# Kernel optimization log

Measured on AMD Instinct MI355X. Metric: run time of the kernel, lower is better.

## Reference

```python
import jax, jax.numpy as jnp
import numpy as np

D_MODEL = 1024
NUM_HEADS = 16
D_K = D_MODEL // NUM_HEADS


def setup_inputs() -> dict:
    key = jax.random.key(0)
    ks = jax.random.split(key, 5)
    s = 1.0 / np.sqrt(D_MODEL)
    return {
        "x": jax.random.normal(ks[0], (2, 2048, D_MODEL), dtype=jnp.float32),
        "Wq": jax.random.normal(ks[1], (D_MODEL, D_MODEL), dtype=jnp.float32) * s,
        "bq": jnp.zeros((D_MODEL,), jnp.float32),
        "Wk": jax.random.normal(ks[2], (D_MODEL, D_MODEL), dtype=jnp.float32) * s,
        "bk": jnp.zeros((D_MODEL,), jnp.float32),
        "Wv": jax.random.normal(ks[3], (D_MODEL, D_MODEL), dtype=jnp.float32) * s,
        "bv": jnp.zeros((D_MODEL,), jnp.float32),
        "Wo": jax.random.normal(ks[4], (D_MODEL, D_MODEL), dtype=jnp.float32) * s,
        "bo": jnp.zeros((D_MODEL,), jnp.float32),
    }


def _rotate_half(t):
    t1, t2 = t[..., : D_K // 2], t[..., D_K // 2 :]
    return jnp.concatenate((-t2, t1), axis=-1)


def reference(x, Wq, bq, Wk, bk, Wv, bv, Wo, bo):
    B, S, D = x.shape
    H, dk = NUM_HEADS, D_K
    # RoPE tables: inv_freq over even dims, emb = cat(freqs, freqs)
    inv_freq = 1.0 / (10000.0 ** (jnp.arange(0, dk, 2, dtype=jnp.float32) / dk))
    pos = jnp.arange(S, dtype=jnp.float32)
    freqs = pos[:, None] * inv_freq[None, :]            # [S, dk/2]
    emb = jnp.concatenate((freqs, freqs), axis=-1)      # [S, dk]
    cos = jnp.cos(emb)[None, :, None, :]                # [1, S, 1, dk]
    sin = jnp.sin(emb)[None, :, None, :]

    q = (x @ Wq + bq).reshape(B, S, H, dk)
    k = (x @ Wk + bk).reshape(B, S, H, dk)
    v = (x @ Wv + bv).reshape(B, S, H, dk)

    q = q * cos + _rotate_half(q) * sin
    k = k * cos + _rotate_half(k) * sin

    # [B,H,S,S] scores, stable softmax, then weighted sum of V
    scores = jnp.einsum("bqhd,bkhd->bhqk", q, k) / jnp.sqrt(jnp.float32(dk))
    attn = jax.nn.softmax(scores, axis=-1)
    out = jnp.einsum("bhqk,bkhd->bqhd", attn, v).reshape(B, S, D)
    return out @ Wo + bo
```

## Files before the change

### kernel.cpp

```cpp
#include <hip/hip_runtime.h>
#include <hip/hip_bf16.h>
#include <math.h>

typedef __bf16 bf16_t;
typedef bf16_t bf16x4 __attribute__((ext_vector_type(4)));
typedef bf16_t bf16x8 __attribute__((ext_vector_type(8)));
typedef float f32x4 __attribute__((ext_vector_type(4)));

#define SEQ 2048
#define BATCH 2
#define NHEAD 16
#define DK 64
#define DMODEL 1024

#define GLOAD16(gsrc, ldst)                                                        \
    __builtin_amdgcn_global_load_lds(                                              \
        (const __attribute__((address_space(1))) void*)(gsrc),                     \
        (__attribute__((address_space(3))) void*)(ldst), 16, 0, 0)

__device__ __forceinline__ float exp2_hw(float x) {
#if __has_builtin(__builtin_amdgcn_exp2f)
    return __builtin_amdgcn_exp2f(x);
#else
    float r; asm("v_exp_f32 %0, %1" : "=v"(r) : "v"(x)); return r;
#endif
}

__global__ __launch_bounds__(256)
void prep_kernel(const float* __restrict__ x, bf16_t* __restrict__ y,
                 const float* __restrict__ W0, const float* __restrict__ W1,
                 const float* __restrict__ W2, const float* __restrict__ W3,
                 bf16_t* __restrict__ Wt, float2* __restrict__ cs) {
    __shared__ float t[32][33];
    const int id = blockIdx.x, tid = threadIdx.x;
    if (id < 4096) {
        int i = (id * 256 + tid) * 4;
        float4 v = *reinterpret_cast<const float4*>(x + i);
        bf16x4 o = { (bf16_t)v.x, (bf16_t)v.y, (bf16_t)v.z, (bf16_t)v.w };
        *reinterpret_cast<bf16x4*>(y + i) = o;
    } else if (id < 8192) {
        const int id2 = id - 4096;
        const int z = id2 >> 10, rem = id2 & 1023;
        const int n0 = (rem & 31) * 32, k0 = ((rem >> 5) & 31) * 32;
        const int tx = tid & 31, ty = tid >> 5;
        const float* W = (z == 0) ? W0 : (z == 1) ? W1 : (z == 2) ? W2 : W3;
        bf16_t* out = Wt + ((size_t)z << 20);
#pragma unroll
        for (int i = 0; i < 32; i += 8)
            t[ty + i][tx] = W[(size_t)(k0 + ty + i) * DMODEL + n0 + tx];
        __syncthreads();
#pragma unroll
        for (int i = 0; i < 32; i += 8)
            out[(size_t)(n0 + ty + i) * DMODEL + k0 + tx] = (bf16_t)t[tx][ty + i];
    } else {
        int idx = (id - 8192) * 256 + tid;
        int j = idx & 31, s = idx >> 5;
        float inv = powf(10000.0f, -(float)j / 32.0f);
        float ang = (float)s * inv;
        cs[idx] = make_float2(cosf(ang), sinf(ang));
    }
}

template<int NF>
__device__ __forceinline__ void gemm_core(const bf16_t* __restrict__ A,
                                          const bf16_t* __restrict__ Bt,
                                          int m0, int n0,
                                          bf16_t* As, bf16_t* Bs,
                                          f32x4 (&acc)[4][NF]) {
    const int tid = threadIdx.x, lane = tid & 63, wid = tid >> 6;
    const int wr = wid >> 1, wc = wid & 1;
    const int lm = lane & 15, lq = lane >> 4;
    constexpr int BROWS = NF * 32;
    constexpr int NT = DMODEL / 32;

    const int r_in = lane >> 2;
    const int csw  = (((lane & 3) ^ ((lane >> 3) & 3)) << 3);
    const bf16_t* Ag = A  + (size_t)(m0 + 32 * wid + r_in) * DMODEL + csw;
    const bf16_t* Bg = Bt + (size_t)(n0 + (NF * 8) * wid + r_in) * DMODEL + csw;
    const int cswr = ((lq ^ ((lm >> 1) & 3)) << 4);

    auto stage = [&](int t, int buf) {
        const int k0 = t * 32;
        bf16_t* a = As + buf * (128 * 32) + 32 * wid * 32;
        bf16_t* b = Bs + buf * (BROWS * 32) + (NF * 8) * wid * 32;
        GLOAD16(Ag + k0,               a);
        GLOAD16(Ag + 16 * DMODEL + k0, a + 16 * 32);
        GLOAD16(Bg + k0,               b);
        if constexpr (NF == 4) GLOAD16(Bg + 16 * DMODEL + k0, b + 16 * 32);
    };

    stage(0, 0);
    stage(1, 1);
    int cb = 0;
    for (int t = 0; t < NT; ++t) {
        if (t + 2 < NT) {
            int sb = cb + 2; if (sb >= 3) sb -= 3;
            stage(t + 2, sb);
            if constexpr (NF == 4) asm volatile("s_waitcnt vmcnt(8)" ::: "memory");
            else                   asm volatile("s_waitcnt vmcnt(6)" ::: "memory");
        } else if (t + 1 < NT) {
            if constexpr (NF == 4) asm volatile("s_waitcnt vmcnt(4)" ::: "memory");
            else                   asm volatile("s_waitcnt vmcnt(3)" ::: "memory");
        } else {
            asm volatile("s_waitcnt vmcnt(0)" ::: "memory");
        }
        __builtin_amdgcn_s_barrier();

        const char* pAs = (const char*)(As + cb * (128 * 32));
        const char* pBs = (const char*)(Bs + cb * (BROWS * 32));
        bf16x8 af[4], bfr[NF];
#pragma unroll
        for (int mf = 0; mf < 4; ++mf)
            af[mf] = *reinterpret_cast<const bf16x8*>(pAs + (wr * 64 + mf * 16 + lm) * 64 + cswr);
#pragma unroll
        for (int nf = 0; nf < NF; ++nf)
            bfr[nf] = *reinterpret_cast<const bf16x8*>(pBs + (wc * (NF * 16) + nf * 16 + lm) * 64 + cswr);
#pragma unroll
        for (int mf = 0; mf < 4; ++mf)
#pragma unroll
            for (int nf = 0; nf < NF; ++nf)
                acc[mf][nf] = __builtin_amdgcn_mfma_f32_16x16x32_bf16(af[mf], bfr[nf], acc[mf][nf], 0, 0, 0);

        asm volatile("" ::: "memory");
        __builtin_amdgcn_s_barrier();
        if (++cb == 3) cb = 0;
    }
}

__global__ __launch_bounds__(256)
void gemm_qkv_kernel(const bf16_t* __restrict__ xb, const bf16_t* __restrict__ wtqk,
                     const bf16_t* __restrict__ wtv,
                     const float* __restrict__ bq, const float* __restrict__ bk,
                     const float* __restrict__ bv,
                     bf16_t* __restrict__ qb, bf16_t* __restrict__ kb,
                     bf16_t* __restrict__ vtb, const float2* __restrict__ cs) {
    __shared__ bf16_t As[3 * 128 * 32];
    __shared__ bf16_t Bs[3 * 128 * 32];
    const int tid = threadIdx.x, lane = tid & 63, wid = tid >> 6;
    const int wr = wid >> 1, wc = wid & 1;
    const int lm = lane & 15, lq = lane >> 4;
    const int orig = blockIdx.x;
    const int id = (orig & 7) * 96 + (orig >> 3);
    f32x4 acc[4][4] = {};

    if (id < 512) {
        const int m0 = (id >> 4) * 128, n0 = (id & 15) * 128;
        gemm_core<4>(xb, wtqk, m0, n0, As, Bs, acc);
        const bool is_k = (n0 >= 1024);
        const float* bs = is_k ? bk : bq;
        bf16_t* C = is_k ? kb : qb;
        const int cb = (is_k ? n0 - 1024 : n0) + wc * 64;
        const float b0 = bs[cb + lm],      b1 = bs[cb + 16 + lm];
        const float b2 = bs[cb + 32 + lm], b3 = bs[cb + 48 + lm];
#pragma unroll
        for (int mf = 0; mf < 4; ++mf)
#pragma unroll
            for (int i = 0; i < 4; ++i) {
                const int row = m0 + wr * 64 + mf * 16 + lq * 4 + i;
                const int s = row & (SEQ - 1);
                const float2 cs0 = cs[s * 32 + lm];
                const float2 cs1 = cs[s * 32 + 16 + lm];
                const float a0 = acc[mf][0][i] + b0, a1 = acc[mf][1][i] + b1;
                const float a2 = acc[mf][2][i] + b2, a3 = acc[mf][3][i] + b3;
                bf16_t* p = C + (size_t)row * DMODEL + cb;
                p[lm]      = (bf16_t)(a0 * cs0.x - a2 * cs0.y);
                p[16 + lm] = (bf16_t)(a1 * cs1.x - a3 * cs1.y);
                p[32 + lm] = (bf16_t)(a2 * cs0.x + a0 * cs0.y);
                p[48 + lm] = (bf16_t)(a3 * cs1.x + a1 * cs1.y);
            }
    } else {
        const int id2 = id - 512;
        const int m0 = (id2 & 7) * 128, n0 = (id2 >> 3) * 128;
        gemm_core<4>(wtv, xb, m0, n0, As, Bs, acc);
#pragma unroll
        for (int mf = 0; mf < 4; ++mf)
#pragma unroll
            for (int i = 0; i < 4; ++i) {
                const int row = m0 + wr * 64 + mf * 16 + lq * 4 + i;
                const float brow = bv[row];
#pragma unroll
                for (int nf = 0; nf < 4; ++nf) {
                    const int col = n0 + wc * 64 + nf * 16 + lm;
                    vtb[(size_t)row * 4096 + col] = (bf16_t)(acc[mf][nf][i] + brow);
                }
            }
    }
}

__global__ __launch_bounds__(256)
void gemm_out_kernel(const bf16_t* __restrict__ A, const bf16_t* __restrict__ Bt,
                     const float* __restrict__ bias, float* __restrict__ C) {
    __shared__ bf16_t As[3 * 128 * 32];
    __shared__ bf16_t Bs[3 * 64 * 32];
    const int tid = threadIdx.x, lane = tid & 63, wid = tid >> 6;
    const int wr = wid >> 1, wc = wid & 1;
    const int lm = lane & 15, lq = lane >> 4;
    const int orig = blockIdx.x;
    const int id = (orig & 7) * 64 + (orig >> 3);
    const int m0 = (id >> 4) * 128, n0 = (id & 15) * 64;
    f32x4 acc[4][2] = {};
    gemm_core<2>(A, Bt, m0, n0, As, Bs, acc);
#pragma unroll
    for (int nf = 0; nf < 2; ++nf) {
        const int col = n0 + wc * 32 + nf * 16 + lm;
        const float bcol = bias[col];
#pragma unroll
        for (int mf = 0; mf < 4; ++mf)
#pragma unroll
            for (int i = 0; i < 4; ++i) {
                const int row = m0 + wr * 64 + mf * 16 + lq * 4 + i;
                C[(size_t)row * DMODEL + col] = acc[mf][nf][i] + bcol;
            }
    }
}

__global__ __launch_bounds__(256)
void attn_kernel(const bf16_t* __restrict__ q, const bf16_t* __restrict__ k,
                 const bf16_t* __restrict__ vt, bf16_t* __restrict__ attnout) {
    const int tid = threadIdx.x, lane = tid & 63, wid = tid >> 6;
    const int lm = lane & 15, lq = lane >> 4;
    const int bid = blockIdx.x;
    const int xcd = bid & 7, idx = bid >> 3;
    const int bh = xcd * 4 + (idx & 3), qblk = idx >> 2;
    const int b = bh >> 4, h = bh & 15;
    const int qrow0 = qblk * 128 + wid * 32;
    const float MS = 20.0f;
    constexpr int NT = SEQ / 64;

    __shared__ bf16_t Ks[4][64][64];
    __shared__ bf16_t Vs[4][64][64];

    const bf16_t* qA = q + ((size_t)(b * SEQ + qrow0 + lm) * NHEAD + h) * DK + lq * 8;
    const bf16_t* qB = qA + (size_t)16 * NHEAD * DK;
    bf16x8 aqA0 = *reinterpret_cast<const bf16x8*>(qA);
    bf16x8 aqA1 = *reinterpret_cast<const bf16x8*>(qA + 32);
    bf16x8 aqB0 = *reinterpret_cast<const bf16x8*>(qB);
    bf16x8 aqB1 = *reinterpret_cast<const bf16x8*>(qB + 32);
#pragma unroll
    for (int j = 0; j < 8; ++j) {
        aqA0[j] = (bf16_t)((float)aqA0[j] * 0.18033688f);
        aqA1[j] = (bf16_t)((float)aqA1[j] * 0.18033688f);
        aqB0[j] = (bf16_t)((float)aqB0[j] * 0.18033688f);
        aqB1[j] = (bf16_t)((float)aqB1[j] * 0.18033688f);
    }
    const bf16_t one = (bf16_t)1.0f;
    const bf16x8 ones = { one, one, one, one, one, one, one, one };
    const f32x4 cinit = { -MS, -MS, -MS, -MS };

    const int r0   = 8 * wid + (lane >> 3);
    const int scol = (((lane & 7) ^ (lane >> 3)) << 3);
    const int sig  = ((r0 >> 2) & 3) * 8 + ((r0 >> 4) & 1) * 4 + (r0 & 3);
    const bf16_t* kg = k  + ((size_t)(b * SEQ + sig) * NHEAD + h) * DK + scol;
    const bf16_t* vg = vt + ((size_t)(h * DK + r0)) * 4096 + (size_t)b * SEQ + scol;
    const size_t kstep = (size_t)NHEAD * DK;
    const char* ksb = (const char*)Ks;
    const char* vsb = (const char*)Vs;
    const int c0 = (lq << 4) ^ ((lm & 7) << 4);
    const int rowb = lm * 128;

    f32x4 OA[4] = {}, OB[4] = {};
    f32x4 olA = {}, olB = {};

    auto stageK = [&](int buf, int kb) {
        GLOAD16(kg + (size_t)kb * kstep,        &Ks[buf][8 * wid][0]);
        GLOAD16(kg + (size_t)(kb + 32) * kstep, &Ks[buf][32 + 8 * wid][0]);
    };
    auto stageV = [&](int buf, int kb) {
        GLOAD16(vg + kb,                        &Vs[buf][8 * wid][0]);
        GLOAD16(vg + (size_t)32 * 4096 + kb,    &Vs[buf][32 + 8 * wid][0]);
    };
    auto qk = [&](int buf, f32x4 (&sA)[4], f32x4 (&sB)[4]) {
        const char* kt = ksb + buf * 8192;
        __builtin_amdgcn_s_setprio(1);
#pragma unroll
        for (int t = 0; t < 4; ++t) {
            bf16x8 a0 = *reinterpret_cast<const bf16x8*>(kt + t * 2048 + rowb + c0);
            bf16x8 a1 = *reinterpret_cast<const bf16x8*>(kt + t * 2048 + rowb + (c0 ^ 64));
            f32x4 xA = __builtin_amdgcn_mfma_f32_16x16x32_bf16(a0, aqA0, cinit, 0, 0, 0);
            xA = __builtin_amdgcn_mfma_f32_16x16x32_bf16(a1, aqA1, xA, 0, 0, 0);
            f32x4 xB = __builtin_amdgcn_mfma_f32_16x16x32_bf16(a0, aqB0, cinit, 0, 0, 0);
            xB = __builtin_amdgcn_mfma_f32_16x16x32_bf16(a1, aqB1, xB, 0, 0, 0);
            sA[t] = xA; sB[t] = xB;
        }
        __builtin_amdgcn_s_setprio(0);
    };
    auto softmax = [&](const f32x4 (&sA)[4], const f32x4 (&sB)[4],
                       bf16x8& pA0, bf16x8& pA1, bf16x8& pB0, bf16x8& pB1) {
#pragma unroll
        for (int u = 0; u < 2; ++u)
#pragma unroll
            for (int i = 0; i < 4; ++i) {
                pA0[4 * u + i] = (bf16_t)exp2_hw(sA[u][i]);
                pA1[4 * u + i] = (bf16_t)exp2_hw(sA[u + 2][i]);
                pB0[4 * u + i] = (bf16_t)exp2_hw(sB[u][i]);
                pB1[4 * u + i] = (bf16_t)exp2_hw(sB[u + 2][i]);
            }
    };
    auto pv = [&](int buf, const bf16x8& pA0, const bf16x8& pA1,
                  const bf16x8& pB0, const bf16x8& pB1) {
        const char* vtl = vsb + buf * 8192;
        __builtin_amdgcn_s_setprio(1);
#pragma unroll
        for (int nf = 0; nf < 4; ++nf) {
            bf16x8 v0 = *reinterpret_cast<const bf16x8*>(vtl + nf * 2048 + rowb + c0);
            bf16x8 v1 = *reinterpret_cast<const bf16x8*>(vtl + nf * 2048 + rowb + (c0 ^ 64));
            f32x4 oA = OA[nf], oB = OB[nf];
            oA = __builtin_amdgcn_mfma_f32_16x16x32_bf16(v0, pA0, oA, 0, 0, 0);
            oA = __builtin_amdgcn_mfma_f32_16x16x32_bf16(v1, pA1, oA, 0, 0, 0);
            oB = __builtin_amdgcn_mfma_f32_16x16x32_bf16(v0, pB0, oB, 0, 0, 0);
            oB = __builtin_amdgcn_mfma_f32_16x16x32_bf16(v1, pB1, oB, 0, 0, 0);
            OA[nf] = oA; OB[nf] = oB;
        }
        olA = __builtin_amdgcn_mfma_f32_16x16x32_bf16(ones, pA0, olA, 0, 0, 0);
        olA = __builtin_amdgcn_mfma_f32_16x16x32_bf16(ones, pA1, olA, 0, 0, 0);
        olB = __builtin_amdgcn_mfma_f32_16x16x32_bf16(ones, pB0, olB, 0, 0, 0);
        olB = __builtin_amdgcn_mfma_f32_16x16x32_bf16(ones, pB1, olB, 0, 0, 0);
        __builtin_amdgcn_s_setprio(0);
    };

    stageK(0, 0);  stageV(0, 0);
    stageK(1, 64); stageV(1, 64);
    asm volatile("s_waitcnt vmcnt(2)" ::: "memory");
    __builtin_amdgcn_s_barrier();
    asm volatile("" ::: "memory");
    f32x4 stA[4], stB[4];
    qk(0, stA, stB);

    const bool evenw = (wid & 1) == 0;
    for (int t = 0; t < NT; ++t) {
        const int kb = t * 64;
        f32x4 nA[4], nB[4];
        bf16x8 paA0, paA1, paB0, paB1;

        if (t + 2 < NT) stageK((t + 2) & 3, kb + 128);
        if (evenw) {
            if (t + 1 < NT) qk((t + 1) & 3, nA, nB);
            if (t + 2 < NT) stageV((t + 2) & 3, kb + 128);
            softmax(stA, stB, paA0, paA1, paB0, paB1);
            pv(t & 3, paA0, paA1, paB0, paB1);
        } else {
            softmax(stA, stB, paA0, paA1, paB0, paB1);
            pv(t & 3, paA0, paA1, paB0, paB1);
            if (t + 2 < NT) stageV((t + 2) & 3, kb + 128);
            if (t + 1 < NT) qk((t + 1) & 3, nA, nB);
        }

        if (t + 1 < NT) {
            if (t + 2 < NT) asm volatile("s_waitcnt vmcnt(2)" ::: "memory");
            else            asm volatile("s_waitcnt vmcnt(0)" ::: "memory");
            __builtin_amdgcn_s_barrier();
            asm volatile("" ::: "memory");
#pragma unroll
            for (int i = 0; i < 4; ++i) { stA[i] = nA[i]; stB[i] = nB[i]; }
        }
    }

    const float invA = 1.0f / olA[0];
    const float invB = 1.0f / olB[0];
    bf16_t* obA = attnout + ((size_t)(b * SEQ + qrow0 + lm) * NHEAD + h) * DK;
    bf16_t* obB = obA + (size_t)16 * NHEAD * DK;
#pragma unroll
    for (int nf = 0; nf < 4; ++nf) {
        bf16x4 cA = { (bf16_t)(OA[nf][0] * invA), (bf16_t)(OA[nf][1] * invA),
                      (bf16_t)(OA[nf][2] * invA), (bf16_t)(OA[nf][3] * invA) };
        bf16x4 cB = { (bf16_t)(OB[nf][0] * invB), (bf16_t)(OB[nf][1] * invB),
                      (bf16_t)(OB[nf][2] * invB), (bf16_t)(OB[nf][3] * invB) };
        *reinterpret_cast<bf16x4*>(obA + nf * 16 + lq * 4) = cA;
        *reinterpret_cast<bf16x4*>(obB + nf * 16 + lq * 4) = cB;
    }
}

extern "C" void kernel_launch(void* const* d_in, const int* in_sizes, int n_in,
                              void* d_out, int out_size, void* d_ws, size_t ws_size,
                              hipStream_t stream) {
    const float* x  = (const float*)d_in[0];
    const float* Wq = (const float*)d_in[1];
    const float* bq = (const float*)d_in[2];
    const float* Wk = (const float*)d_in[3];
    const float* bk = (const float*)d_in[4];
    const float* Wv = (const float*)d_in[5];
    const float* bv = (const float*)d_in[6];
    const float* Wo = (const float*)d_in[7];
    const float* bo = (const float*)d_in[8];
    float* out = (float*)d_out;

    char* ws = (char*)d_ws;
    bf16_t* xb  = (bf16_t*)(ws);
    bf16_t* wtq = (bf16_t*)(ws + ((size_t)8  << 20));
    bf16_t* wtv = wtq + (2 << 20);
    bf16_t* wto = wtq + (3 << 20);
    bf16_t* qb  = (bf16_t*)(ws + ((size_t)16 << 20));
    bf16_t* kb  = (bf16_t*)(ws + ((size_t)24 << 20));
    bf16_t* vtb = (bf16_t*)(ws + ((size_t)32 << 20));
    float2* csT = (float2*)(ws + ((size_t)40 << 20));
    bf16_t* aob = xb;

    prep_kernel<<<8448, 256, 0, stream>>>(x, xb, Wq, Wk, Wv, Wo, wtq, csT);
    gemm_qkv_kernel<<<768, 256, 0, stream>>>(xb, wtq, wtv, bq, bk, bv, qb, kb, vtb, csT);
    attn_kernel<<<512, 256, 0, stream>>>(qb, kb, vtb, aob);
    gemm_out_kernel<<<512, 256, 0, stream>>>(aob, wto, bo, out);
}
```

Measured before the change: 120.8 us.

## Use 256x256 tiles with 8-wave blocks for QKV GEMM; widen out-projection tiles

The QKV projection moves to a new 512-thread kernel that computes 256x256 output tiles with a 64-deep K step and double-buffered LDS staged in halves. This raises arithmetic intensity and cuts global/LDS traffic per FLOP. The output projection goes from 128x64 to 128x128 tiles, halving its grid to 256 blocks. The cost is fewer blocks (192 and 256), which may underfill the 256 CUs, plus higher register pressure from the 8x4 accumulators.

```diff
diff --git a/kernel.cpp b/kernel.cpp
--- a/kernel.cpp
+++ b/kernel.cpp
@@ -17,6 +17,8 @@
     __builtin_amdgcn_global_load_lds(                                              \
         (const __attribute__((address_space(1))) void*)(gsrc),                     \
         (__attribute__((address_space(3))) void*)(ldst), 16, 0, 0)
+
+#define MFMA16(a, b, c) __builtin_amdgcn_mfma_f32_16x16x32_bf16((a), (b), (c), 0, 0, 0)
 
 __device__ __forceinline__ float exp2_hw(float x) {
 #if __has_builtin(__builtin_amdgcn_exp2f)
@@ -61,6 +63,134 @@
     }
 }
 
+__global__ __launch_bounds__(512)
+void gemm_qkv8_kernel(const bf16_t* __restrict__ xb, const bf16_t* __restrict__ wtqk,
+                      const bf16_t* __restrict__ wtv,
+                      const float* __restrict__ bq, const float* __restrict__ bk,
+                      const float* __restrict__ bv,
+                      bf16_t* __restrict__ qb, bf16_t* __restrict__ kb,
+                      bf16_t* __restrict__ vtb, const float2* __restrict__ cs) {
+    __shared__ bf16_t As[2][2][128 * 64];
+    __shared__ bf16_t Bs[2][2][128 * 64];
+    const int tid = threadIdx.x, lane = tid & 63, wid = tid >> 6;
+    const int wm = wid >> 2, wn = wid & 3;
+    const int lm = lane & 15, lq = lane >> 4;
+    const int orig = blockIdx.x;
+    const int id = (orig & 7) * 24 + (orig >> 3);
+    const bool isV = (id >= 128);
+    const int id2 = isV ? id - 128 : id;
+    const int m0 = isV ? (id2 & 3) * 256 : (id2 >> 3) * 256;
+    const int n0 = isV ? (id2 >> 2) * 256 : (id2 & 7) * 256;
+    const bf16_t* Amat = isV ? wtv : xb;
+    const bf16_t* Bmat = isV ? xb : wtqk;
+
+    const int scol = (((lane & 7) ^ (lane >> 3)) << 3);
+    const int srow = wid * 8 + (lane >> 3);
+
+    auto stageH = [&](int idx, int kt) {
+        const int buf = kt & 1, h = idx & 1;
+        const bf16_t* g; bf16_t* d;
+        if (idx < 2) { g = Amat + (size_t)(m0 + h * 128 + srow) * DMODEL + kt * 64 + scol;
+                       d = &As[buf][h][wid * 512]; }
+        else         { g = Bmat + (size_t)(n0 + h * 128 + srow) * DMODEL + kt * 64 + scol;
+                       d = &Bs[buf][h][wid * 512]; }
+        GLOAD16(g, d);
+        GLOAD16(g + (size_t)64 * DMODEL, d + 4096);
+    };
+
+    f32x4 acc[8][4] = {};
+    const int rB = (wn & 1) * 64;
+    const int xsw = (lm & 7) << 4;
+
+    stageH(0, 0); stageH(1, 0); stageH(2, 0); stageH(3, 0);
+
+    constexpr int NT = DMODEL / 64;
+    for (int kt = 0; kt < NT; ++kt) {
+        const char* pA = (const char*)&As[kt & 1][wm][0];
+        const char* pB = (const char*)&Bs[kt & 1][wn >> 1][0];
+        bf16x8 bfr[4][2];
+#pragma unroll
+        for (int p = 0; p < 4; ++p) {
+            if (kt + 1 < NT) stageH(p, kt + 1);
+            if (p == 0) {
+                if (kt + 1 < NT) asm volatile("s_waitcnt vmcnt(2)" ::: "memory");
+                else             asm volatile("s_waitcnt vmcnt(0)" ::: "memory");
+            }
+            __builtin_amdgcn_s_barrier();
+            asm volatile("" ::: "memory");
+
+            if (p == 0) {
+#pragma unroll
+                for (int nf = 0; nf < 4; ++nf)
+#pragma unroll
+                    for (int kk = 0; kk < 2; ++kk)
+                        bfr[nf][kk] = *reinterpret_cast<const bf16x8*>(
+                            pB + (rB + nf * 16 + lm) * 128 + (((kk << 6) | (lq << 4)) ^ xsw));
+            }
+            bf16x8 af[2][2];
+#pragma unroll
+            for (int m = 0; m < 2; ++m)
+#pragma unroll
+                for (int kk = 0; kk < 2; ++kk)
+                    af[m][kk] = *reinterpret_cast<const bf16x8*>(
+                        pA + ((2 * p + m) * 16 + lm) * 128 + (((kk << 6) | (lq << 4)) ^ xsw));
+
+            __builtin_amdgcn_s_setprio(1);
+#pragma unroll
+            for (int m = 0; m < 2; ++m)
+#pragma unroll
+                for (int nf = 0; nf < 4; ++nf) {
+                    f32x4 o = acc[2 * p + m][nf];
+                    o = MFMA16(af[m][0], bfr[nf][0], o);
+                    o = MFMA16(af[m][1], bfr[nf][1], o);
+                    acc[2 * p + m][nf] = o;
+                }
+            __builtin_amdgcn_s_setprio(0);
+            asm volatile("" ::: "memory");
+            __builtin_amdgcn_s_barrier();
+        }
+    }
+
+    if (!isV) {
+        const int cba = n0 + wn * 64;
+        const bool is_k = (cba >= 1024);
+        const float* bs = is_k ? bk : bq;
+        bf16_t* C = is_k ? kb : qb;
+        const int cb = is_k ? cba - 1024 : cba;
+        const float b0 = bs[cb + lm],      b1 = bs[cb + 16 + lm];
+        const float b2 = bs[cb + 32 + lm], b3 = bs[cb + 48 + lm];
+#pragma unroll
+        for (int mf = 0; mf < 8; ++mf)
+#pragma unroll
+            for (int i = 0; i < 4; ++i) {
+                const int row = m0 + wm * 128 + mf * 16 + lq * 4 + i;
+                const int s = row & (SEQ - 1);
+                const float2 cs0 = cs[s * 32 + lm];
+                const float2 cs1 = cs[s * 32 + 16 + lm];
+                const float a0 = acc[mf][0][i] + b0, a1 = acc[mf][1][i] + b1;
+                const float a2 = acc[mf][2][i] + b2, a3 = acc[mf][3][i] + b3;
+                bf16_t* p = C + (size_t)row * DMODEL + cb;
+                p[lm]      = (bf16_t)(a0 * cs0.x - a2 * cs0.y);
+                p[16 + lm] = (bf16_t)(a1 * cs1.x - a3 * cs1.y);
+                p[32 + lm] = (bf16_t)(a2 * cs0.x + a0 * cs0.y);
+                p[48 + lm] = (bf16_t)(a3 * cs1.x + a1 * cs1.y);
+            }
+    } else {
+#pragma unroll
+        for (int mf = 0; mf < 8; ++mf)
+#pragma unroll
+            for (int i = 0; i < 4; ++i) {
+                const int row = m0 + wm * 128 + mf * 16 + lq * 4 + i;
+                const float brow = bv[row];
+#pragma unroll
+                for (int nf = 0; nf < 4; ++nf) {
+                    const int col = n0 + wn * 64 + nf * 16 + lm;
+                    vtb[(size_t)row * 4096 + col] = (bf16_t)(acc[mf][nf][i] + brow);
+                }
+            }
+    }
+}
+
 template<int NF>
 __device__ __forceinline__ void gemm_core(const bf16_t* __restrict__ A,
                                           const bf16_t* __restrict__ Bt,
@@ -119,7 +249,7 @@
         for (int mf = 0; mf < 4; ++mf)
 #pragma unroll
             for (int nf = 0; nf < NF; ++nf)
-                acc[mf][nf] = __builtin_amdgcn_mfma_f32_16x16x32_bf16(af[mf], bfr[nf], acc[mf][nf], 0, 0, 0);
+                acc[mf][nf] = MFMA16(af[mf], bfr[nf], acc[mf][nf]);
 
         asm volatile("" ::: "memory");
         __builtin_amdgcn_s_barrier();
@@ -128,81 +258,21 @@
 }
 
 __global__ __launch_bounds__(256)
-void gemm_qkv_kernel(const bf16_t* __restrict__ xb, const bf16_t* __restrict__ wtqk,
-                     const bf16_t* __restrict__ wtv,
-                     const float* __restrict__ bq, const float* __restrict__ bk,
-                     const float* __restrict__ bv,
-                     bf16_t* __restrict__ qb, bf16_t* __restrict__ kb,
-                     bf16_t* __restrict__ vtb, const float2* __restrict__ cs) {
+void gemm_out_kernel(const bf16_t* __restrict__ A, const bf16_t* __restrict__ Bt,
+                     const float* __restrict__ bias, float* __restrict__ C) {
     __shared__ bf16_t As[3 * 128 * 32];
     __shared__ bf16_t Bs[3 * 128 * 32];
     const int tid = threadIdx.x, lane = tid & 63, wid = tid >> 6;
     const int wr = wid >> 1, wc = wid & 1;
     const int lm = lane & 15, lq = lane >> 4;
     const int orig = blockIdx.x;
-    const int id = (orig & 7) * 96 + (orig >> 3);
+    const int id = (orig & 7) * 32 + (orig >> 3);
+    const int m0 = (id >> 3) * 128, n0 = (id & 7) * 128;
     f32x4 acc[4][4] = {};
-
-    if (id < 512) {
-        const int m0 = (id >> 4) * 128, n0 = (id & 15) * 128;
-        gemm_core<4>(xb, wtqk, m0, n0, As, Bs, acc);
-        const bool is_k = (n0 >= 1024);
-        const float* bs = is_k ? bk : bq;
-        bf16_t* C = is_k ? kb : qb;
-        const int cb = (is_k ? n0 - 1024 : n0) + wc * 64;
-        const float b0 = bs[cb + lm],      b1 = bs[cb + 16 + lm];
-        const float b2 = bs[cb + 32 + lm], b3 = bs[cb + 48 + lm];
-#pragma unroll
-        for (int mf = 0; mf < 4; ++mf)
-#pragma unroll
-            for (int i = 0; i < 4; ++i) {
-                const int row = m0 + wr * 64 + mf * 16 + lq * 4 + i;
-                const int s = row & (SEQ - 1);
-                const float2 cs0 = cs[s * 32 + lm];
-                const float2 cs1 = cs[s * 32 + 16 + lm];
-                const float a0 = acc[mf][0][i] + b0, a1 = acc[mf][1][i] + b1;
-                const float a2 = acc[mf][2][i] + b2, a3 = acc[mf][3][i] + b3;
-                bf16_t* p = C + (size_t)row * DMODEL + cb;
-                p[lm]      = (bf16_t)(a0 * cs0.x - a2 * cs0.y);
-                p[16 + lm] = (bf16_t)(a1 * cs1.x - a3 * cs1.y);
-                p[32 + lm] = (bf16_t)(a2 * cs0.x + a0 * cs0.y);
-                p[48 + lm] = (bf16_t)(a3 * cs1.x + a1 * cs1.y);
-            }
-    } else {
-        const int id2 = id - 512;
-        const int m0 = (id2 & 7) * 128, n0 = (id2 >> 3) * 128;
-        gemm_core<4>(wtv, xb, m0, n0, As, Bs, acc);
-#pragma unroll
-        for (int mf = 0; mf < 4; ++mf)
-#pragma unroll
-            for (int i = 0; i < 4; ++i) {
-                const int row = m0 + wr * 64 + mf * 16 + lq * 4 + i;
-                const float brow = bv[row];
-#pragma unroll
-                for (int nf = 0; nf < 4; ++nf) {
-                    const int col = n0 + wc * 64 + nf * 16 + lm;
-                    vtb[(size_t)row * 4096 + col] = (bf16_t)(acc[mf][nf][i] + brow);
-                }
-            }
-    }
-}
-
-__global__ __launch_bounds__(256)
-void gemm_out_kernel(const bf16_t* __restrict__ A, const bf16_t* __restrict__ Bt,
-                     const float* __restrict__ bias, float* __restrict__ C) {
-    __shared__ bf16_t As[3 * 128 * 32];
-    __shared__ bf16_t Bs[3 * 64 * 32];
-    const int tid = threadIdx.x, lane = tid & 63, wid = tid >> 6;
-    const int wr = wid >> 1, wc = wid & 1;
-    const int lm = lane & 15, lq = lane >> 4;
-    const int orig = blockIdx.x;
-    const int id = (orig & 7) * 64 + (orig >> 3);
-    const int m0 = (id >> 4) * 128, n0 = (id & 15) * 64;
-    f32x4 acc[4][2] = {};
-    gemm_core<2>(A, Bt, m0, n0, As, Bs, acc);
-#pragma unroll
-    for (int nf = 0; nf < 2; ++nf) {
-        const int col = n0 + wc * 32 + nf * 16 + lm;
+    gemm_core<4>(A, Bt, m0, n0, As, Bs, acc);
+#pragma unroll
+    for (int nf = 0; nf < 4; ++nf) {
+        const int col = n0 + wc * 64 + nf * 16 + lm;
         const float bcol = bias[col];
 #pragma unroll
         for (int mf = 0; mf < 4; ++mf)
@@ -276,10 +346,10 @@
         for (int t = 0; t < 4; ++t) {
             bf16x8 a0 = *reinterpret_cast<const bf16x8*>(kt + t * 2048 + rowb + c0);
             bf16x8 a1 = *reinterpret_cast<const bf16x8*>(kt + t * 2048 + rowb + (c0 ^ 64));
-            f32x4 xA = __builtin_amdgcn_mfma_f32_16x16x32_bf16(a0, aqA0, cinit, 0, 0, 0);
-            xA = __builtin_amdgcn_mfma_f32_16x16x32_bf16(a1, aqA1, xA, 0, 0, 0);
-            f32x4 xB = __builtin_amdgcn_mfma_f32_16x16x32_bf16(a0, aqB0, cinit, 0, 0, 0);
-            xB = __builtin_amdgcn_mfma_f32_16x16x32_bf16(a1, aqB1, xB, 0, 0, 0);
+            f32x4 xA = MFMA16(a0, aqA0, cinit);
+            xA = MFMA16(a1, aqA1, xA);
+            f32x4 xB = MFMA16(a0, aqB0, cinit);
+            xB = MFMA16(a1, aqB1, xB);
             sA[t] = xA; sB[t] = xB;
         }
         __builtin_amdgcn_s_setprio(0);
@@ -305,16 +375,16 @@
             bf16x8 v0 = *reinterpret_cast<const bf16x8*>(vtl + nf * 2048 + rowb + c0);
             bf16x8 v1 = *reinterpret_cast<const bf16x8*>(vtl + nf * 2048 + rowb + (c0 ^ 64));
             f32x4 oA = OA[nf], oB = OB[nf];
-            oA = __builtin_amdgcn_mfma_f32_16x16x32_bf16(v0, pA0, oA, 0, 0, 0);
-            oA = __builtin_amdgcn_mfma_f32_16x16x32_bf16(v1, pA1, oA, 0, 0, 0);
-            oB = __builtin_amdgcn_mfma_f32_16x16x32_bf16(v0, pB0, oB, 0, 0, 0);
-            oB = __builtin_amdgcn_mfma_f32_16x16x32_bf16(v1, pB1, oB, 0, 0, 0);
+            oA = MFMA16(v0, pA0, oA);
+            oA = MFMA16(v1, pA1, oA);
+            oB = MFMA16(v0, pB0, oB);
+            oB = MFMA16(v1, pB1, oB);
             OA[nf] = oA; OB[nf] = oB;
         }
-        olA = __builtin_amdgcn_mfma_f32_16x16x32_bf16(ones, pA0, olA, 0, 0, 0);
-        olA = __builtin_amdgcn_mfma_f32_16x16x32_bf16(ones, pA1, olA, 0, 0, 0);
-        olB = __builtin_amdgcn_mfma_f32_16x16x32_bf16(ones, pB0, olB, 0, 0, 0);
-        olB = __builtin_amdgcn_mfma_f32_16x16x32_bf16(ones, pB1, olB, 0, 0, 0);
+        olA = MFMA16(ones, pA0, olA);
+        olA = MFMA16(ones, pA1, olA);
+        olB = MFMA16(ones, pB0, olB);
+        olB = MFMA16(ones, pB1, olB);
         __builtin_amdgcn_s_setprio(0);
     };
 
@@ -396,7 +466,7 @@
     bf16_t* aob = xb;
 
     prep_kernel<<<8448, 256, 0, stream>>>(x, xb, Wq, Wk, Wv, Wo, wtq, csT);
-    gemm_qkv_kernel<<<768, 256, 0, stream>>>(xb, wtq, wtv, bq, bk, bv, qb, kb, vtb, csT);
+    gemm_qkv8_kernel<<<192, 512, 0, stream>>>(xb, wtq, wtv, bq, bk, bv, qb, kb, vtb, csT);
     attn_kernel<<<512, 256, 0, stream>>>(qb, kb, vtb, aob);
-    gemm_out_kernel<<<512, 256, 0, stream>>>(aob, wto, bo, out);
-}
+    gemm_out_kernel<<<256, 256, 0, stream>>>(aob, wto, bo, out);
+}
```

Result: slower. 130.9 us (+8.4%).

## Use 128-key double-buffered attention tiles and 128x128 output GEMM tiles

Applied to the files above, without the earlier changes.

The attention kernel now stages 128 keys per step into two K/V buffers instead of 64 keys into four buffers. Each step processes two 64-key halves, and the staging loads are issued after a barrier, so there are half as many barrier rounds. The K/V staging addresses and swizzles are recomputed for the new layout. The output projection GEMM moves from 128x64 to 128x128 tiles with 256 blocks, which raises per-block reuse but lowers block count and parallelism, and the new pipeline has less prefetch lookahead than the old four-buffer scheme.

```diff
diff --git a/kernel.cpp b/kernel.cpp
--- a/kernel.cpp
+++ b/kernel.cpp
@@ -17,6 +17,8 @@
     __builtin_amdgcn_global_load_lds(                                              \
         (const __attribute__((address_space(1))) void*)(gsrc),                     \
         (__attribute__((address_space(3))) void*)(ldst), 16, 0, 0)
+
+#define MFMA16(a, b, c) __builtin_amdgcn_mfma_f32_16x16x32_bf16((a), (b), (c), 0, 0, 0)
 
 __device__ __forceinline__ float exp2_hw(float x) {
 #if __has_builtin(__builtin_amdgcn_exp2f)
@@ -119,7 +121,7 @@
         for (int mf = 0; mf < 4; ++mf)
 #pragma unroll
             for (int nf = 0; nf < NF; ++nf)
-                acc[mf][nf] = __builtin_amdgcn_mfma_f32_16x16x32_bf16(af[mf], bfr[nf], acc[mf][nf], 0, 0, 0);
+                acc[mf][nf] = MFMA16(af[mf], bfr[nf], acc[mf][nf]);
 
         asm volatile("" ::: "memory");
         __builtin_amdgcn_s_barrier();
@@ -191,18 +193,18 @@
 void gemm_out_kernel(const bf16_t* __restrict__ A, const bf16_t* __restrict__ Bt,
                      const float* __restrict__ bias, float* __restrict__ C) {
     __shared__ bf16_t As[3 * 128 * 32];
-    __shared__ bf16_t Bs[3 * 64 * 32];
+    __shared__ bf16_t Bs[3 * 128 * 32];
     const int tid = threadIdx.x, lane = tid & 63, wid = tid >> 6;
     const int wr = wid >> 1, wc = wid & 1;
     const int lm = lane & 15, lq = lane >> 4;
     const int orig = blockIdx.x;
-    const int id = (orig & 7) * 64 + (orig >> 3);
-    const int m0 = (id >> 4) * 128, n0 = (id & 15) * 64;
-    f32x4 acc[4][2] = {};
-    gemm_core<2>(A, Bt, m0, n0, As, Bs, acc);
-#pragma unroll
-    for (int nf = 0; nf < 2; ++nf) {
-        const int col = n0 + wc * 32 + nf * 16 + lm;
+    const int id = (orig & 7) * 32 + (orig >> 3);
+    const int m0 = (id >> 3) * 128, n0 = (id & 7) * 128;
+    f32x4 acc[4][4] = {};
+    gemm_core<4>(A, Bt, m0, n0, As, Bs, acc);
+#pragma unroll
+    for (int nf = 0; nf < 4; ++nf) {
+        const int col = n0 + wc * 64 + nf * 16 + lm;
         const float bcol = bias[col];
 #pragma unroll
         for (int mf = 0; mf < 4; ++mf)
@@ -225,10 +227,10 @@
     const int b = bh >> 4, h = bh & 15;
     const int qrow0 = qblk * 128 + wid * 32;
     const float MS = 20.0f;
-    constexpr int NT = SEQ / 64;
-
-    __shared__ bf16_t Ks[4][64][64];
-    __shared__ bf16_t Vs[4][64][64];
+    constexpr int NT = SEQ / 128;
+
+    __shared__ bf16_t Ks[2][128][64];
+    __shared__ bf16_t Vs[2][64][128];
 
     const bf16_t* qA = q + ((size_t)(b * SEQ + qrow0 + lm) * NHEAD + h) * DK + lq * 8;
     const bf16_t* qB = qA + (size_t)16 * NHEAD * DK;
@@ -247,39 +249,52 @@
     const bf16x8 ones = { one, one, one, one, one, one, one, one };
     const f32x4 cinit = { -MS, -MS, -MS, -MS };
 
-    const int r0   = 8 * wid + (lane >> 3);
-    const int scol = (((lane & 7) ^ (lane >> 3)) << 3);
-    const int sig  = ((r0 >> 2) & 3) * 8 + ((r0 >> 4) & 1) * 4 + (r0 & 3);
-    const bf16_t* kg = k  + ((size_t)(b * SEQ + sig) * NHEAD + h) * DK + scol;
-    const bf16_t* vg = vt + ((size_t)(h * DK + r0)) * 4096 + (size_t)b * SEQ + scol;
+    const int rr = lane >> 3;
+    const int scolK = (((lane & 7) ^ rr) << 3);
     const size_t kstep = (size_t)NHEAD * DK;
+    const bf16_t* kgc[4];
+#pragma unroll
+    for (int c = 0; c < 4; ++c) {
+        const int row = 32 * wid + 8 * c + rr;
+        const int half = row >> 6, r6 = row & 63;
+        const int sigr = (r6 & 32) | (((r6 >> 2) & 3) << 3) | (((r6 >> 4) & 1) << 2) | (r6 & 3);
+        kgc[c] = k + ((size_t)(b * SEQ + half * 64 + sigr) * NHEAD + h) * DK + scolK;
+    }
+    const bf16_t* vgc[4];
+#pragma unroll
+    for (int c = 0; c < 4; ++c) {
+        const int d = 16 * wid + 4 * c + (lane >> 4);
+        const int g = lane & 15, half128 = g >> 3, gin = g & 7;
+        const int colsrc = half128 * 64 + ((gin ^ (d & 7)) << 3);
+        vgc[c] = vt + ((size_t)(h * DK + d)) * 4096 + (size_t)b * SEQ + colsrc;
+    }
+
     const char* ksb = (const char*)Ks;
     const char* vsb = (const char*)Vs;
     const int c0 = (lq << 4) ^ ((lm & 7) << 4);
-    const int rowb = lm * 128;
+    const int rowbK = lm * 128;
 
     f32x4 OA[4] = {}, OB[4] = {};
     f32x4 olA = {}, olB = {};
 
-    auto stageK = [&](int buf, int kb) {
-        GLOAD16(kg + (size_t)kb * kstep,        &Ks[buf][8 * wid][0]);
-        GLOAD16(kg + (size_t)(kb + 32) * kstep, &Ks[buf][32 + 8 * wid][0]);
+    auto stage = [&](int buf, int kb) {
+#pragma unroll
+        for (int c = 0; c < 4; ++c) {
+            GLOAD16(kgc[c] + (size_t)kb * kstep, &Ks[buf][32 * wid + 8 * c][0]);
+            GLOAD16(vgc[c] + kb,                 &Vs[buf][16 * wid + 4 * c][0]);
+        }
     };
-    auto stageV = [&](int buf, int kb) {
-        GLOAD16(vg + kb,                        &Vs[buf][8 * wid][0]);
-        GLOAD16(vg + (size_t)32 * 4096 + kb,    &Vs[buf][32 + 8 * wid][0]);
-    };
-    auto qk = [&](int buf, f32x4 (&sA)[4], f32x4 (&sB)[4]) {
-        const char* kt = ksb + buf * 8192;
+    auto qk = [&](int buf, int sub, f32x4 (&sA)[4], f32x4 (&sB)[4]) {
+        const char* kt = ksb + buf * 16384 + sub * 8192;
         __builtin_amdgcn_s_setprio(1);
 #pragma unroll
         for (int t = 0; t < 4; ++t) {
-            bf16x8 a0 = *reinterpret_cast<const bf16x8*>(kt + t * 2048 + rowb + c0);
-            bf16x8 a1 = *reinterpret_cast<const bf16x8*>(kt + t * 2048 + rowb + (c0 ^ 64));
-            f32x4 xA = __builtin_amdgcn_mfma_f32_16x16x32_bf16(a0, aqA0, cinit, 0, 0, 0);
-            xA = __builtin_amdgcn_mfma_f32_16x16x32_bf16(a1, aqA1, xA, 0, 0, 0);
-            f32x4 xB = __builtin_amdgcn_mfma_f32_16x16x32_bf16(a0, aqB0, cinit, 0, 0, 0);
-            xB = __builtin_amdgcn_mfma_f32_16x16x32_bf16(a1, aqB1, xB, 0, 0, 0);
+            bf16x8 a0 = *reinterpret_cast<const bf16x8*>(kt + t * 2048 + rowbK + c0);
+            bf16x8 a1 = *reinterpret_cast<const bf16x8*>(kt + t * 2048 + rowbK + (c0 ^ 64));
+            f32x4 xA = MFMA16(a0, aqA0, cinit);
+            xA = MFMA16(a1, aqA1, xA);
+            f32x4 xB = MFMA16(a0, aqB0, cinit);
+            xB = MFMA16(a1, aqB1, xB);
             sA[t] = xA; sB[t] = xB;
         }
         __builtin_amdgcn_s_setprio(0);
@@ -296,62 +311,68 @@
                 pB1[4 * u + i] = (bf16_t)exp2_hw(sB[u + 2][i]);
             }
     };
-    auto pv = [&](int buf, const bf16x8& pA0, const bf16x8& pA1,
+    auto pv = [&](int buf, int sub, const bf16x8& pA0, const bf16x8& pA1,
                   const bf16x8& pB0, const bf16x8& pB1) {
-        const char* vtl = vsb + buf * 8192;
+        const char* vtl = vsb + buf * 16384;
         __builtin_amdgcn_s_setprio(1);
 #pragma unroll
         for (int nf = 0; nf < 4; ++nf) {
-            bf16x8 v0 = *reinterpret_cast<const bf16x8*>(vtl + nf * 2048 + rowb + c0);
-            bf16x8 v1 = *reinterpret_cast<const bf16x8*>(vtl + nf * 2048 + rowb + (c0 ^ 64));
+            const char* vr = vtl + nf * 4096 + lm * 256 + sub * 128;
+            bf16x8 v0 = *reinterpret_cast<const bf16x8*>(vr + c0);
+            bf16x8 v1 = *reinterpret_cast<const bf16x8*>(vr + (c0 ^ 64));
             f32x4 oA = OA[nf], oB = OB[nf];
-            oA = __builtin_amdgcn_mfma_f32_16x16x32_bf16(v0, pA0, oA, 0, 0, 0);
-            oA = __builtin_amdgcn_mfma_f32_16x16x32_bf16(v1, pA1, oA, 0, 0, 0);
-            oB = __builtin_amdgcn_mfma_f32_16x16x32_bf16(v0, pB0, oB, 0, 0, 0);
-            oB = __builtin_amdgcn_mfma_f32_16x16x32_bf16(v1, pB1, oB, 0, 0, 0);
+            oA = MFMA16(v0, pA0, oA);
+            oA = MFMA16(v1, pA1, oA);
+            oB = MFMA16(v0, pB0, oB);
+            oB = MFMA16(v1, pB1, oB);
             OA[nf] = oA; OB[nf] = oB;
         }
-        olA = __builtin_amdgcn_mfma_f32_16x16x32_bf16(ones, pA0, olA, 0, 0, 0);
-        olA = __builtin_amdgcn_mfma_f32_16x16x32_bf16(ones, pA1, olA, 0, 0, 0);
-        olB = __builtin_amdgcn_mfma_f32_16x16x32_bf16(ones, pB0, olB, 0, 0, 0);
-        olB = __builtin_amdgcn_mfma_f32_16x16x32_bf16(ones, pB1, olB, 0, 0, 0);
+        olA = MFMA16(ones, pA0, olA);
+        olA = MFMA16(ones, pA1, olA);
+        olB = MFMA16(ones, pB0, olB);
+        olB = MFMA16(ones, pB1, olB);
         __builtin_amdgcn_s_setprio(0);
     };
 
-    stageK(0, 0);  stageV(0, 0);
-    stageK(1, 64); stageV(1, 64);
-    asm volatile("s_waitcnt vmcnt(2)" ::: "memory");
+    stage(0, 0);
+    stage(1, 128);
+    asm volatile("s_waitcnt vmcnt(8)" ::: "memory");
     __builtin_amdgcn_s_barrier();
     asm volatile("" ::: "memory");
+
     f32x4 stA[4], stB[4];
-    qk(0, stA, stB);
+    qk(0, 0, stA, stB);
 
     const bool evenw = (wid & 1) == 0;
     for (int t = 0; t < NT; ++t) {
-        const int kb = t * 64;
+        const int buf = t & 1;
         f32x4 nA[4], nB[4];
         bf16x8 paA0, paA1, paB0, paB1;
 
-        if (t + 2 < NT) stageK((t + 2) & 3, kb + 128);
         if (evenw) {
-            if (t + 1 < NT) qk((t + 1) & 3, nA, nB);
-            if (t + 2 < NT) stageV((t + 2) & 3, kb + 128);
+            qk(buf, 1, nA, nB);
             softmax(stA, stB, paA0, paA1, paB0, paB1);
-            pv(t & 3, paA0, paA1, paB0, paB1);
+            pv(buf, 0, paA0, paA1, paB0, paB1);
         } else {
             softmax(stA, stB, paA0, paA1, paB0, paB1);
-            pv(t & 3, paA0, paA1, paB0, paB1);
-            if (t + 2 < NT) stageV((t + 2) & 3, kb + 128);
-            if (t + 1 < NT) qk((t + 1) & 3, nA, nB);
-        }
+            pv(buf, 0, paA0, paA1, paB0, paB1);
+            qk(buf, 1, nA, nB);
+        }
+        softmax(nA, nB, paA0, paA1, paB0, paB1);
+        pv(buf, 1, paA0, paA1, paB0, paB1);
 
         if (t + 1 < NT) {
-            if (t + 2 < NT) asm volatile("s_waitcnt vmcnt(2)" ::: "memory");
-            else            asm volatile("s_waitcnt vmcnt(0)" ::: "memory");
+            asm volatile("" ::: "memory");
+            __builtin_amdgcn_s_barrier();
+            if (t + 2 < NT) {
+                stage(buf, (t + 2) * 128);
+                asm volatile("s_waitcnt vmcnt(8)" ::: "memory");
+            } else {
+                asm volatile("s_waitcnt vmcnt(0)" ::: "memory");
+            }
             __builtin_amdgcn_s_barrier();
             asm volatile("" ::: "memory");
-#pragma unroll
-            for (int i = 0; i < 4; ++i) { stA[i] = nA[i]; stB[i] = nB[i]; }
+            qk((t + 1) & 1, 0, stA, stB);
         }
     }
 
@@ -398,5 +419,5 @@
     prep_kernel<<<8448, 256, 0, stream>>>(x, xb, Wq, Wk, Wv, Wo, wtq, csT);
     gemm_qkv_kernel<<<768, 256, 0, stream>>>(xb, wtq, wtv, bq, bk, bv, qb, kb, vtb, csT);
     attn_kernel<<<512, 256, 0, stream>>>(qb, kb, vtb, aob);
-    gemm_out_kernel<<<512, 256, 0, stream>>>(aob, wto, bo, out);
-}
+    gemm_out_kernel<<<256, 256, 0, stream>>>(aob, wto, bo, out);
+}
```

New measurement: 123.8 us. +2.5%, slower.
